# Performance work log

Hardware: AMD Instinct MI355X
Metric: run time of the kernel (lower is better)

## Reference

```python
import jax, jax.numpy as jnp
import numpy as np

N_EXPERTS = 8


def setup_inputs() -> dict:
    key = jax.random.key(0)
    k_x, k_e, k_r = jax.random.split(key, 3)
    N, D = 262144, 256
    inputs = jax.random.normal(k_x, (N, D), dtype=jnp.float32)
    # nn.Linear(dim, dim, bias=False) weight: [out, in]; stacked per expert -> [8, D, D]
    scale = 1.0 / np.sqrt(D)
    w_experts = jax.random.uniform(k_e, (N_EXPERTS, D, D), dtype=jnp.float32,
                                   minval=-scale, maxval=scale)
    # router: Linear(dim, 1, bias=False) weight -> [1, D]
    w_router = jax.random.uniform(k_r, (1, D), dtype=jnp.float32,
                                  minval=-scale, maxval=scale)
    return {"inputs": inputs, "w_experts": w_experts, "w_router": w_router}


def reference(inputs, w_experts, w_router):
    # gate_logits: [N, 1]; topk(k=1) over last dim of size 1 -> selected expert is
    # always index 0 (faithful to the original module's degenerate routing).
    gate_logits = inputs @ w_router.T                      # [N, 1]
    selected = jnp.argmax(gate_logits, axis=-1)            # [N], all zeros structurally
    # (softmaxed `weights` in the original are computed but never used -> omitted)
    results = jnp.zeros_like(inputs)
    for i in range(N_EXPERTS):
        mask = (selected == i).astype(inputs.dtype)[:, None]  # [N, 1]
        results = results + mask * (inputs @ w_experts[i].T)  # masked dispatch-combine
    return results
```

## Files before the change

kernel.cpp:

```cpp
#include <hip/hip_runtime.h>
#include <hip/hip_bf16.h>

typedef __attribute__((ext_vector_type(4))) float  f32x4;
typedef __attribute__((ext_vector_type(8))) short  bf16x8;
typedef __attribute__((ext_vector_type(4))) short  bf16x4;

#define DIM       256
#define NBLOCKS   256
#define NTHREADS  512
#define NROUNDS   16
#define CBASE     65536
#define LDS_BYTES 131072

#define WAITV(N) asm volatile("s_waitcnt vmcnt(" #N ")" ::: "memory")

__device__ __forceinline__ short f2bf(float x) {
    __hip_bfloat16 h = __float2bfloat16(x);
    return *reinterpret_cast<short*>(&h);
}

__device__ __forceinline__ f32x4 gload4(const float* p) {
    f32x4 r;
    asm volatile("global_load_dwordx4 %0, %1, off" : "=v"(r) : "v"(p) : "memory");
    return r;
}

__global__ __launch_bounds__(NTHREADS, 2)
void moe_expert0_kernel(const float* __restrict__ X,
                        const float* __restrict__ W0,
                        float* __restrict__ Out)
{
    extern __shared__ char lds[];
    const int tid  = threadIdx.x;
    const int lane = tid & 63;
    const int wave = tid >> 6;
    const int b    = blockIdx.x;

    #pragma unroll
    for (int i = 0; i < 16; ++i) {
        int chunk = tid + i * NTHREADS;
        int row = chunk >> 5;
        int c8  = chunk & 31;
        const f32x4* src = reinterpret_cast<const f32x4*>(W0 + row * DIM + c8 * 8);
        f32x4 f0 = src[0], f1 = src[1];
        bf16x8 w;
        w[0] = f2bf(f0[0]); w[1] = f2bf(f0[1]); w[2] = f2bf(f0[2]); w[3] = f2bf(f0[3]);
        w[4] = f2bf(f1[0]); w[5] = f2bf(f1[1]); w[6] = f2bf(f1[2]); w[7] = f2bf(f1[3]);
        int addr = row * 512 + ((c8 * 16) ^ ((row & 15) << 4));
        *reinterpret_cast<bf16x8*>(lds + addr) = w;
    }
    asm volatile("s_waitcnt vmcnt(0) lgkmcnt(0)" ::: "memory");
    __builtin_amdgcn_s_barrier();

    const int l15 = lane & 15;
    const int lg  = lane >> 4;
    const int cg  = wave & 3;
    const int tg  = wave >> 2;

    bf16x8 Breg[4][8];
    #pragma unroll
    for (int nt = 0; nt < 4; ++nt)
        #pragma unroll
        for (int s = 0; s < 8; ++s)
            Breg[nt][s] = *reinterpret_cast<const bf16x8*>(
                lds + (cg * 64 + nt * 16 + l15) * 512 + ((s * 64 + lg * 16) ^ (l15 << 4)));
    asm volatile("s_waitcnt lgkmcnt(0)" ::: "memory");
    __builtin_amdgcn_s_barrier();

    const int srow = wave * 8;
    const float* Xblk = X + (size_t)b * 1024 * DIM;
    float*       Oblk = Out + (size_t)b * 1024 * DIM;

    f32x4 Xrow[8];
    #define ALOAD(R) do {                                                      \
        int rr_ = (R) > NROUNDS - 1 ? NROUNDS - 1 : (R);                       \
        _Pragma("unroll")                                                      \
        for (int jj = 0; jj < 8; ++jj)                                         \
            Xrow[jj] = gload4(Xblk + (size_t)(rr_ * 64 + srow + jj) * DIM      \
                              + lane * 4);                                     \
    } while (0)
    #define ASTORE(BUF) do {                                                   \
        _Pragma("unroll")                                                      \
        for (int jj = 0; jj < 8; ++jj) {                                       \
            int row_ = srow + jj;                                              \
            f32x4 xv = Xrow[jj];                                               \
            bf16x4 xw;                                                         \
            xw[0] = f2bf(xv[0]); xw[1] = f2bf(xv[1]);                          \
            xw[2] = f2bf(xv[2]); xw[3] = f2bf(xv[3]);                          \
            int dst = (BUF) * 32768 + row_ * 512                               \
                    + ((((lane >> 1) ^ (row_ & 15)) << 4)) + (lane & 1) * 8;   \
            *reinterpret_cast<bf16x4*>(lds + dst) = xw;                        \
        }                                                                      \
    } while (0)

    ALOAD(0);
    WAITV(0); __builtin_amdgcn_sched_barrier(0);
    ASTORE(0);
    ALOAD(1);
    asm volatile("s_waitcnt lgkmcnt(0)" ::: "memory");
    __builtin_amdgcn_s_barrier();

    for (int r = 0; r < NROUNDS; ++r) {
        const char* ab = lds + (r & 1) * 32768;

        f32x4 acc[2][4];
        #pragma unroll
        for (int mt = 0; mt < 2; ++mt)
            #pragma unroll
            for (int nt = 0; nt < 4; ++nt) acc[mt][nt] = (f32x4)0.0f;

        #pragma unroll
        for (int s = 0; s < 8; ++s) {
            bf16x8 a0 = *reinterpret_cast<const bf16x8*>(
                ab + (tg * 32 + l15) * 512      + ((s * 64 + lg * 16) ^ (l15 << 4)));
            bf16x8 a1 = *reinterpret_cast<const bf16x8*>(
                ab + (tg * 32 + 16 + l15) * 512 + ((s * 64 + lg * 16) ^ (l15 << 4)));
            #pragma unroll
            for (int nt = 0; nt < 4; ++nt) {
                acc[0][nt] = __builtin_amdgcn_mfma_f32_16x16x32_bf16(Breg[nt][s], a0, acc[0][nt], 0, 0, 0);
                acc[1][nt] = __builtin_amdgcn_mfma_f32_16x16x32_bf16(Breg[nt][s], a1, acc[1][nt], 0, 0, 0);
            }
        }

        #pragma unroll
        for (int mt = 0; mt < 2; ++mt)
            #pragma unroll
            for (int nt = 0; nt < 4; ++nt) {
                int row_ = tg * 32 + mt * 16 + l15;
                int sc   = cg * 16 + nt * 4 + lg;
                int dst  = CBASE + row_ * 1024 + ((sc ^ (row_ & 7)) << 4);
                *reinterpret_cast<f32x4*>(lds + dst) = acc[mt][nt];
            }

        if (r + 1 < NROUNDS) {
            if (r) { WAITV(8); } else { WAITV(0); }
            __builtin_amdgcn_sched_barrier(0);
            ASTORE((r + 1) & 1);
            ALOAD(r + 2);
        }
        asm volatile("s_waitcnt lgkmcnt(0)" ::: "memory");
        __builtin_amdgcn_s_barrier();

        #pragma unroll
        for (int jj = 0; jj < 8; ++jj) {
            int row_ = srow + jj;
            f32x4 v = *reinterpret_cast<const f32x4*>(
                lds + CBASE + row_ * 1024 + ((lane << 4) ^ ((row_ & 7) << 4)));
            __builtin_nontemporal_store(v, reinterpret_cast<f32x4*>(
                Oblk + (size_t)(r * 64 + row_) * DIM + lane * 4));
        }
        asm volatile("" ::: "memory");
        __builtin_amdgcn_s_barrier();
    }
    WAITV(0);
    #undef ALOAD
    #undef ASTORE
}

extern "C" void kernel_launch(void* const* d_in, const int* in_sizes, int n_in,
                              void* d_out, int out_size, void* d_ws, size_t ws_size,
                              hipStream_t stream) {
    (void)in_sizes; (void)n_in; (void)d_ws; (void)ws_size; (void)out_size;
    const float* X = (const float*)d_in[0];
    const float* W = (const float*)d_in[1];
    float* Out = (float*)d_out;

    hipFuncSetAttribute((const void*)moe_expert0_kernel,
                        hipFuncAttributeMaxDynamicSharedMemorySize, LDS_BYTES);
    moe_expert0_kernel<<<dim3(NBLOCKS), dim3(NTHREADS), LDS_BYTES, stream>>>(X, W, Out);
}
```

Before: 91.29 us.

## Halve per-block tile and LDS to double block count and occupancy

```diff
diff --git a/kernel.cpp b/kernel.cpp
--- a/kernel.cpp
+++ b/kernel.cpp
@@ -6,11 +6,12 @@
 typedef __attribute__((ext_vector_type(4))) short  bf16x4;
 
 #define DIM       256
-#define NBLOCKS   256
+#define NBLOCKS   512
 #define NTHREADS  512
+#define TOKPB     512
 #define NROUNDS   16
-#define CBASE     65536
-#define LDS_BYTES 131072
+#define CBASE     32768
+#define LDS_BYTES 65536
 
 #define WAITV(N) asm volatile("s_waitcnt vmcnt(" #N ")" ::: "memory")
 
@@ -36,22 +37,6 @@
     const int wave = tid >> 6;
     const int b    = blockIdx.x;
 
-    #pragma unroll
-    for (int i = 0; i < 16; ++i) {
-        int chunk = tid + i * NTHREADS;
-        int row = chunk >> 5;
-        int c8  = chunk & 31;
-        const f32x4* src = reinterpret_cast<const f32x4*>(W0 + row * DIM + c8 * 8);
-        f32x4 f0 = src[0], f1 = src[1];
-        bf16x8 w;
-        w[0] = f2bf(f0[0]); w[1] = f2bf(f0[1]); w[2] = f2bf(f0[2]); w[3] = f2bf(f0[3]);
-        w[4] = f2bf(f1[0]); w[5] = f2bf(f1[1]); w[6] = f2bf(f1[2]); w[7] = f2bf(f1[3]);
-        int addr = row * 512 + ((c8 * 16) ^ ((row & 15) << 4));
-        *reinterpret_cast<bf16x8*>(lds + addr) = w;
-    }
-    asm volatile("s_waitcnt vmcnt(0) lgkmcnt(0)" ::: "memory");
-    __builtin_amdgcn_s_barrier();
-
     const int l15 = lane & 15;
     const int lg  = lane >> 4;
     const int cg  = wave & 3;
@@ -59,35 +44,56 @@
 
     bf16x8 Breg[4][8];
     #pragma unroll
-    for (int nt = 0; nt < 4; ++nt)
+    for (int c = 0; c < 4; ++c) {
         #pragma unroll
-        for (int s = 0; s < 8; ++s)
-            Breg[nt][s] = *reinterpret_cast<const bf16x8*>(
-                lds + (cg * 64 + nt * 16 + l15) * 512 + ((s * 64 + lg * 16) ^ (l15 << 4)));
-    asm volatile("s_waitcnt lgkmcnt(0)" ::: "memory");
-    __builtin_amdgcn_s_barrier();
+        for (int i = 0; i < 4; ++i) {
+            int chunk = tid + i * NTHREADS;
+            int lrow  = chunk >> 5;
+            int c8    = chunk & 31;
+            const f32x4* src = reinterpret_cast<const f32x4*>(
+                W0 + (size_t)(c * 64 + lrow) * DIM + c8 * 8);
+            f32x4 f0 = src[0], f1 = src[1];
+            bf16x8 w;
+            w[0] = f2bf(f0[0]); w[1] = f2bf(f0[1]); w[2] = f2bf(f0[2]); w[3] = f2bf(f0[3]);
+            w[4] = f2bf(f1[0]); w[5] = f2bf(f1[1]); w[6] = f2bf(f1[2]); w[7] = f2bf(f1[3]);
+            int addr = lrow * 512 + ((c8 * 16) ^ ((lrow & 15) << 4));
+            *reinterpret_cast<bf16x8*>(lds + addr) = w;
+        }
+        asm volatile("s_waitcnt vmcnt(0) lgkmcnt(0)" ::: "memory");
+        __builtin_amdgcn_s_barrier();
+        if (cg == c) {
+            #pragma unroll
+            for (int nt = 0; nt < 4; ++nt)
+                #pragma unroll
+                for (int s = 0; s < 8; ++s)
+                    Breg[nt][s] = *reinterpret_cast<const bf16x8*>(
+                        lds + (nt * 16 + l15) * 512 + ((s * 64 + lg * 16) ^ (l15 << 4)));
+            asm volatile("s_waitcnt lgkmcnt(0)" ::: "memory");
+        }
+        __builtin_amdgcn_s_barrier();
+    }
 
-    const int srow = wave * 8;
-    const float* Xblk = X + (size_t)b * 1024 * DIM;
-    float*       Oblk = Out + (size_t)b * 1024 * DIM;
+    const int srow4 = wave * 4;
+    const float* Xblk = X + (size_t)b * TOKPB * DIM;
+    float*       Oblk = Out + (size_t)b * TOKPB * DIM;
 
-    f32x4 Xrow[8];
+    f32x4 Xrow[4];
     #define ALOAD(R) do {                                                      \
         int rr_ = (R) > NROUNDS - 1 ? NROUNDS - 1 : (R);                       \
         _Pragma("unroll")                                                      \
-        for (int jj = 0; jj < 8; ++jj)                                         \
-            Xrow[jj] = gload4(Xblk + (size_t)(rr_ * 64 + srow + jj) * DIM      \
+        for (int jj = 0; jj < 4; ++jj)                                         \
+            Xrow[jj] = gload4(Xblk + (size_t)(rr_ * 32 + srow4 + jj) * DIM     \
                               + lane * 4);                                     \
     } while (0)
     #define ASTORE(BUF) do {                                                   \
         _Pragma("unroll")                                                      \
-        for (int jj = 0; jj < 8; ++jj) {                                       \
-            int row_ = srow + jj;                                              \
+        for (int jj = 0; jj < 4; ++jj) {                                       \
+            int row_ = srow4 + jj;                                             \
             f32x4 xv = Xrow[jj];                                               \
             bf16x4 xw;                                                         \
             xw[0] = f2bf(xv[0]); xw[1] = f2bf(xv[1]);                          \
             xw[2] = f2bf(xv[2]); xw[3] = f2bf(xv[3]);                          \
-            int dst = (BUF) * 32768 + row_ * 512                               \
+            int dst = (BUF) * 16384 + row_ * 512                               \
                     + ((((lane >> 1) ^ (row_ & 15)) << 4)) + (lane & 1) * 8;   \
             *reinterpret_cast<bf16x4*>(lds + dst) = xw;                        \
         }                                                                      \
@@ -101,39 +107,31 @@
     __builtin_amdgcn_s_barrier();
 
     for (int r = 0; r < NROUNDS; ++r) {
-        const char* ab = lds + (r & 1) * 32768;
+        const char* ab = lds + (r & 1) * 16384;
 
-        f32x4 acc[2][4];
+        f32x4 acc[4];
         #pragma unroll
-        for (int mt = 0; mt < 2; ++mt)
-            #pragma unroll
-            for (int nt = 0; nt < 4; ++nt) acc[mt][nt] = (f32x4)0.0f;
+        for (int nt = 0; nt < 4; ++nt) acc[nt] = (f32x4)0.0f;
 
         #pragma unroll
         for (int s = 0; s < 8; ++s) {
             bf16x8 a0 = *reinterpret_cast<const bf16x8*>(
-                ab + (tg * 32 + l15) * 512      + ((s * 64 + lg * 16) ^ (l15 << 4)));
-            bf16x8 a1 = *reinterpret_cast<const bf16x8*>(
-                ab + (tg * 32 + 16 + l15) * 512 + ((s * 64 + lg * 16) ^ (l15 << 4)));
+                ab + (tg * 16 + l15) * 512 + ((s * 64 + lg * 16) ^ (l15 << 4)));
             #pragma unroll
-            for (int nt = 0; nt < 4; ++nt) {
-                acc[0][nt] = __builtin_amdgcn_mfma_f32_16x16x32_bf16(Breg[nt][s], a0, acc[0][nt], 0, 0, 0);
-                acc[1][nt] = __builtin_amdgcn_mfma_f32_16x16x32_bf16(Breg[nt][s], a1, acc[1][nt], 0, 0, 0);
-            }
+            for (int nt = 0; nt < 4; ++nt)
+                acc[nt] = __builtin_amdgcn_mfma_f32_16x16x32_bf16(Breg[nt][s], a0, acc[nt], 0, 0, 0);
         }
 
         #pragma unroll
-        for (int mt = 0; mt < 2; ++mt)
-            #pragma unroll
-            for (int nt = 0; nt < 4; ++nt) {
-                int row_ = tg * 32 + mt * 16 + l15;
-                int sc   = cg * 16 + nt * 4 + lg;
-                int dst  = CBASE + row_ * 1024 + ((sc ^ (row_ & 7)) << 4);
-                *reinterpret_cast<f32x4*>(lds + dst) = acc[mt][nt];
-            }
+        for (int nt = 0; nt < 4; ++nt) {
+            int row_ = tg * 16 + l15;
+            int sc   = cg * 16 + nt * 4 + lg;
+            int dst  = CBASE + row_ * 1024 + ((sc ^ (row_ & 7)) << 4);
+            *reinterpret_cast<f32x4*>(lds + dst) = acc[nt];
+        }
 
         if (r + 1 < NROUNDS) {
-            if (r) { WAITV(8); } else { WAITV(0); }
+            if (r) { WAITV(4); } else { WAITV(0); }
             __builtin_amdgcn_sched_barrier(0);
             ASTORE((r + 1) & 1);
             ALOAD(r + 2);
@@ -142,12 +140,12 @@
         __builtin_amdgcn_s_barrier();
 
         #pragma unroll
-        for (int jj = 0; jj < 8; ++jj) {
-            int row_ = srow + jj;
+        for (int jj = 0; jj < 4; ++jj) {
+            int row_ = srow4 + jj;
             f32x4 v = *reinterpret_cast<const f32x4*>(
                 lds + CBASE + row_ * 1024 + ((lane << 4) ^ ((row_ & 7) << 4)));
             __builtin_nontemporal_store(v, reinterpret_cast<f32x4*>(
-                Oblk + (size_t)(r * 64 + row_) * DIM + lane * 4));
+                Oblk + (size_t)(r * 32 + row_) * DIM + lane * 4));
         }
         asm volatile("" ::: "memory");
         __builtin_amdgcn_s_barrier();
```

Result: slower. 97.46 us (+6.8%).
